# Kernel optimization log

Measured on AMD Instinct MI355X. Metric: run time of the kernel, lower is better.

Reference implementation:

```python
import jax, jax.numpy as jnp
import numpy as np

N = 50000
E = 800000
D = 256        # encoder_dim; also hidden*heads for both layers
H = 4          # heads
C = 64         # hidden_dim per head
OUT = 5        # classes
NEG_SLOPE = 0.2
GN_EPS = 1e-5
SM_EPS = 1e-16  # PyG softmax denominator epsilon


def setup_inputs() -> dict:
    key = jax.random.key(0)
    ks = jax.random.split(key, 20)
    sc = lambda fan_in: 1.0 / np.sqrt(fan_in)
    inp = {
        "x": jax.random.normal(ks[0], (N, D), dtype=jnp.float32),
        "edge_index": jax.random.randint(ks[1], (2, E), 0, N, dtype=jnp.int64),
        # two GATv2 layers (stacked on leading axis): lin_l, lin_r, att, bias
        "Wl": jax.random.normal(ks[2], (2, D, H * C), dtype=jnp.float32) * sc(D),
        "Wr": jax.random.normal(ks[3], (2, D, H * C), dtype=jnp.float32) * sc(D),
        "att": jax.random.normal(ks[4], (2, H, C), dtype=jnp.float32) * sc(C),
        "bconv": jnp.zeros((2, H * C), dtype=jnp.float32),
        # parallel linear skips
        "Wlin": jax.random.normal(ks[5], (2, D, H * C), dtype=jnp.float32) * sc(D),
        "blin": jnp.zeros((2, H * C), dtype=jnp.float32),
        # GraphNorm params
        "gn_w": jnp.ones((2, H * C), dtype=jnp.float32),
        "gn_b": jnp.zeros((2, H * C), dtype=jnp.float32),
        "gn_ms": jnp.ones((2, H * C), dtype=jnp.float32),
        # final GATv2 (concat=False -> head mean, out=5) and final linear
        "fWl": jax.random.normal(ks[6], (D, H * OUT), dtype=jnp.float32) * sc(D),
        "fWr": jax.random.normal(ks[7], (D, H * OUT), dtype=jnp.float32) * sc(D),
        "fatt": jax.random.normal(ks[8], (H, OUT), dtype=jnp.float32) * sc(OUT),
        "fbconv": jnp.zeros((OUT,), dtype=jnp.float32),
        "fWlin": jax.random.normal(ks[9], (D, OUT), dtype=jnp.float32) * sc(D),
        "fblin": jnp.zeros((OUT,), dtype=jnp.float32),
    }
    return inp


def _gatv2(x, src, dst, Wl, Wr, att, heads, ch):
    # x: [N, Din]; returns [N, heads, ch]
    n = x.shape[0]
    xl = (x @ Wl).reshape(n, heads, ch)  # source messages
    xr = (x @ Wr).reshape(n, heads, ch)  # target query part
    e = jax.nn.leaky_relu(xl[src] + xr[dst], NEG_SLOPE)      # [E, H, C]
    score = jnp.einsum("ehc,hc->eh", e, att)                  # [E, H]
    # segment softmax over incoming edges of each target node
    m = jax.ops.segment_max(score, dst, num_segments=n)       # [N, H]
    a = jnp.exp(score - m[dst])
    denom = jax.ops.segment_sum(a, dst, num_segments=n)       # [N, H]
    alpha = a / (denom[dst] + SM_EPS)                         # [E, H]
    return jax.ops.segment_sum(alpha[..., None] * xl[src], dst, num_segments=n)


def _graphnorm(x, w, b, ms):
    mean = jnp.mean(x, axis=0)
    centered = x - mean * ms
    var = jnp.mean(centered * centered, axis=0)
    return w * centered * jax.lax.rsqrt(var + GN_EPS) + b


def reference(x, edge_index, Wl, Wr, att, bconv, Wlin, blin, gn_w, gn_b, gn_ms,
              fWl, fWr, fatt, fbconv, fWlin, fblin):
    src, dst = edge_index[0], edge_index[1]
    emb = x
    for i in range(2):
        cpart = _gatv2(emb, src, dst, Wl[i], Wr[i], att[i], H, C).reshape(N, H * C) + bconv[i]
        lpart = emb @ Wlin[i] + blin[i]
        cpart = _graphnorm(cpart, gn_w[i], gn_b[i], gn_ms[i])
        emb = jax.nn.elu(cpart + lpart)
    cpart = _gatv2(emb, src, dst, fWl, fWr, fatt, H, OUT).mean(axis=1) + fbconv  # concat=False
    lpart = emb @ fWlin + fblin
    return jax.nn.log_softmax(cpart + lpart, axis=1)
```

## Files before the change

### kernel.cpp

```cpp
#include <hip/hip_runtime.h>

#define NN 50000
#define EE 800000
#define DD 256
#define NB 196

typedef unsigned short u16;
typedef unsigned int u32;

typedef __attribute__((ext_vector_type(8))) short short8;
typedef __attribute__((ext_vector_type(4))) float f32x4;
typedef __attribute__((ext_vector_type(4))) unsigned short u16x4;
typedef __attribute__((ext_vector_type(4))) int i32x4;

__device__ __forceinline__ float b2f(u16 u) {
  union { u32 i; float f; } c; c.i = ((u32)u) << 16; return c.f;
}
__device__ __forceinline__ u16 f2b(float f) {
  union { float f; u32 i; } c; c.f = f;
  u32 u = c.i;
  return (u16)((u + 0x7fffu + ((u >> 16) & 1u)) >> 16);
}
__device__ __forceinline__ float lrelu(float x) { return fmaxf(x, 0.2f * x); }
__device__ __forceinline__ float ldf(const void* p, int i, int bf) {
  return bf ? b2f(((const u16*)p)[i]) : ((const float*)p)[i];
}
__device__ __forceinline__ int lde(const void* ei, int idx, int m64) {
  int v = m64 ? (int)((const long long*)ei)[idx] : ((const int*)ei)[idx];
  return v < 0 ? 0 : (v >= NN ? NN - 1 : v);
}
__device__ __forceinline__ float cexp(float s) {
  return __expf(__builtin_amdgcn_fmed3f(s, -60.f, 60.f));
}

template <int CTRL>
__device__ __forceinline__ float dpp_add(float s) {
  union { float f; int i; } a, b;
  a.f = s;
  b.i = __builtin_amdgcn_update_dpp(0, a.i, CTRL, 0xf, 0xf, true);
  return s + b.f;
}
__device__ __forceinline__ float row16_allsum(float s) {
  s = dpp_add<0xB1>(s);
  s = dpp_add<0x4E>(s);
  s = dpp_add<0x141>(s);
  s = dpp_add<0x140>(s);
  return s;
}

__device__ __forceinline__ void gload_lds16(const void* g, void* l) {
  __builtin_amdgcn_global_load_lds(
      (const __attribute__((address_space(1))) void*)g,
      (__attribute__((address_space(3))) void*)l, 16, 0, 0);
}

__global__ __launch_bounds__(256) void init_kernel(const void* x, const void* ei,
                                                   int* flags, int* cnt) {
  int i = blockIdx.x * 256 + threadIdx.x;
  if (i < NN) cnt[i] = 0;
  if (blockIdx.x == 0 && threadIdx.x < 64) {
    int lane = threadIdx.x;
    const u16* xw = (const u16*)x;
    int c = 0;
    for (int k = lane; k < 512; k += 64) {
      u16 w = xw[k];
      int e = (w >> 7) & 0xFF;
      if ((e >= 107 && e <= 147) || (w & 0x7FFF) == 0) ++c;
    }
    const u32* ew = (const u32*)ei;
    int zc = 0;
    for (int k = 1 + 2 * lane; k < 1024; k += 128)
      if (ew[k] == 0) ++zc;
    #pragma unroll
    for (int off = 1; off < 64; off <<= 1) {
      c += __shfl_xor(c, off);
      zc += __shfl_xor(zc, off);
    }
    if (lane == 0) {
      flags[0] = (c >= 440) ? 1 : 0;
      flags[1] = (zc >= 400) ? 1 : 0;
    }
  }
}

__global__ void hist_kernel(const void* ei, const int* flags, int* cnt) {
  int e = blockIdx.x * 256 + threadIdx.x;
  if (e < EE) atomicAdd(&cnt[lde(ei, EE + e, flags[1])], 1);
}

__global__ __launch_bounds__(256) void bsum_kernel(const int* __restrict__ deg,
                                                   int* __restrict__ bsum) {
  int i = blockIdx.x * 256 + threadIdx.x;
  int v = (i < NN) ? deg[i] : 0;
  #pragma unroll
  for (int off = 1; off < 64; off <<= 1) v += __shfl_xor(v, off);
  __shared__ int ws[4];
  int lane = threadIdx.x & 63, wid = threadIdx.x >> 6;
  if (lane == 0) ws[wid] = v;
  __syncthreads();
  if (threadIdx.x == 0) bsum[blockIdx.x] = ws[0] + ws[1] + ws[2] + ws[3];
}

__global__ __launch_bounds__(256) void bscan_kernel(const int* __restrict__ bsum,
                                                    int* __restrict__ boff) {
  int t = threadIdx.x;
  int v = (t < NB) ? bsum[t] : 0;
  int iv = v;
  int lane = t & 63, wid = t >> 6;
  #pragma unroll
  for (int off = 1; off < 64; off <<= 1) {
    int u = __shfl_up(iv, off);
    if (lane >= off) iv += u;
  }
  __shared__ int ws[4];
  if (lane == 63) ws[wid] = iv;
  __syncthreads();
  int add = 0;
  for (int w = 0; w < wid; ++w) add += ws[w];
  if (t < NB) boff[t] = iv - v + add;
}

__global__ __launch_bounds__(256) void bwrite_kernel(const int* __restrict__ deg,
                                                     const int* __restrict__ boff,
                                                     int* __restrict__ rowptr) {
  int i = blockIdx.x * 256 + threadIdx.x;
  int v = (i < NN) ? deg[i] : 0;
  int iv = v;
  int lane = threadIdx.x & 63, wid = threadIdx.x >> 6;
  #pragma unroll
  for (int off = 1; off < 64; off <<= 1) {
    int u = __shfl_up(iv, off);
    if (lane >= off) iv += u;
  }
  __shared__ int ws[4];
  if (lane == 63) ws[wid] = iv;
  __syncthreads();
  int add = boff[blockIdx.x];
  for (int w = 0; w < wid; ++w) add += ws[w];
  if (i <= NN) rowptr[i] = iv - v + add;
}

__global__ void fill_kernel(const void* ei, const int* flags, const int* __restrict__ rowptr,
                            int* __restrict__ cnt, int* __restrict__ col) {
  int e = blockIdx.x * 256 + threadIdx.x;
  if (e < EE) {
    int m64 = flags[1];
    int dst = lde(ei, EE + e, m64);
    int old = atomicSub(&cnt[dst], 1);
    int pos = rowptr[dst] + old - 1;
    if (pos >= 0 && pos < EE) col[pos] = lde(ei, e, m64);
  }
}

__global__ __launch_bounds__(256) void prep_kernel(
    const void* Wl, const void* Wr, const void* Wlin,
    const void* fWl, const void* fWr, const void* fWlin,
    const void* x, const int* flags, u16* wpack, u16* fwp, u16* xb) {
  int bf = flags[0];
  int bid = blockIdx.x;
  if (bid < 1536) {
    int idx = bid * 256 + threadIdx.x;
    int m = idx >> 16, e = idx & 65535;
    int layer = (m >= 3) ? 1 : 0, sel = m - layer * 3;
    const void* src = (sel == 0 ? Wl : (sel == 1 ? Wr : Wlin));
    int k = e >> 8, n = e & 255;
    wpack[(m << 16) + ((((k >> 3) << 8) + n) << 3) + (k & 7)] =
        f2b(ldf(src, layer * 65536 + e, bf));
  } else if (bid < 1584) {
    int idx = (bid - 1536) * 256 + threadIdx.x;
    int j = idx & 7;
    int col = (idx >> 3) % 48;
    int kk = idx / (48 * 8);
    int k = kk * 8 + j;
    float v = 0.f;
    if (col < 20)      v = ldf(fWl, k * 20 + col, bf);
    else if (col < 40) v = ldf(fWr, k * 20 + (col - 20), bf);
    else if (col < 45) v = ldf(fWlin, k * 5 + (col - 40), bf);
    fwp[idx] = f2b(v);
  } else {
    int base = (bid - 1584) * 1024 + threadIdx.x * 4;
    if (bf) {
      *(u16x4*)(xb + base) = *(const u16x4*)((const u16*)x + base);
    } else {
      f32x4 s = *(const f32x4*)((const float*)x + base);
      u16x4 o;
      #pragma unroll
      for (int j = 0; j < 4; ++j) o[j] = f2b(s[j]);
      *(u16x4*)(xb + base) = o;
    }
  }
}

__global__ __launch_bounds__(256) void gemm_kernel(
    const u16* __restrict__ A, const u16* __restrict__ wpack, const void* blin,
    const int* flags, int layer, float* __restrict__ sums,
    u16* __restrict__ xl, u16* __restrict__ xr, u16* __restrict__ lp, int M) {
  __shared__ __align__(16) u16 bsh[16384];
  if (blockIdx.x == 0 && blockIdx.y == 0) {
    sums[threadIdx.x] = 0.f;
    sums[threadIdx.x + 256] = 0.f;
  }
  int wave = threadIdx.x >> 6;
  int lane = threadIdx.x & 63;
  int q = lane >> 4;
  int t = lane & 15;
  int m0 = blockIdx.x * 64 + wave * 16;
  int yh = blockIdx.y;

  int arow = m0 + t;
  if (arow >= M) arow = M - 1;
  const u16* Abase = A + (size_t)arow * DD + q * 8;
  short8 af[8];
  #pragma unroll
  for (int i = 0; i < 8; ++i) af[i] = *(const short8*)(Abase + i * 32);

  int bf = flags[0];
  int m = m0 + t;

  for (int yi = 0; yi < 6; ++yi) {
    int y = yh * 6 + yi;
    int mm = y >> 2;
    int col0 = (y & 3) * 64;
    const u16* wb = wpack + (mm << 16);

    __syncthreads();
    #pragma unroll
    for (int itc = 0; itc < 8; ++itc) {
      int kk = wave + itc * 4;
      const u16* gp = wb + (((kk << 8) + col0) << 3) + (lane << 3);
      u16* lb = &bsh[(wave * 64 + itc * 256) << 3];
      gload_lds16(gp, lb);
    }
    __syncthreads();

    f32x4 acc[4];
    #pragma unroll
    for (int ns = 0; ns < 4; ++ns) acc[ns] = (f32x4){0.f, 0.f, 0.f, 0.f};

    #pragma unroll
    for (int i = 0; i < 8; ++i) {
      int kk = i * 4 + q;
      const u16* bb = &bsh[(kk << 9) + (t << 3)];
      #pragma unroll
      for (int ns = 0; ns < 4; ++ns) {
        short8 b = *(const short8*)(bb + (ns << 7));
        acc[ns] = __builtin_amdgcn_mfma_f32_16x16x32_bf16(b, af[i], acc[ns], 0, 0, 0);
      }
    }

    u16* dstp = (y < 4) ? xl : (y < 8) ? xr : lp;
    bool isLp = (y >= 8);
    if (m < M) {
      #pragma unroll
      for (int ns = 0; ns < 4; ++ns) {
        int c0 = col0 + ns * 16 + q * 4;
        u16x4 w;
        #pragma unroll
        for (int r = 0; r < 4; ++r) {
          float bias = isLp ? ldf(blin, layer * 256 + c0 + r, bf) : 0.f;
          w[r] = f2b(acc[ns][r] + bias);
        }
        *(u16x4*)(dstp + (size_t)m * DD + c0) = w;
      }
    }
  }
}

__global__ __launch_bounds__(256) void fgemm_kernel(
    const u16* __restrict__ A, const u16* __restrict__ fwp, const void* fblin,
    const int* flags, float* __restrict__ zl, float* __restrict__ zr,
    float* __restrict__ lp5, int M) {
  int wave = threadIdx.x >> 6;
  int lane = threadIdx.x & 63;
  int q = lane >> 4;
  int t = lane & 15;
  int m0 = blockIdx.x * 64 + wave * 16;

  f32x4 acc[3];
  #pragma unroll
  for (int ns = 0; ns < 3; ++ns) acc[ns] = (f32x4){0.f, 0.f, 0.f, 0.f};

  int arow = m0 + t;
  if (arow >= M) arow = M - 1;
  const u16* Abase = A + (size_t)arow * DD + q * 8;

  #pragma unroll
  for (int k0 = 0; k0 < DD; k0 += 32) {
    short8 a = *(const short8*)(Abase + k0);
    int kk = (k0 >> 3) + q;
    #pragma unroll
    for (int ns = 0; ns < 3; ++ns) {
      short8 b = *(const short8*)(fwp + (((kk * 48) + ns * 16 + t) << 3));
      acc[ns] = __builtin_amdgcn_mfma_f32_16x16x32_bf16(a, b, acc[ns], 0, 0, 0);
    }
  }

  int bf = flags[0];
  #pragma unroll
  for (int ns = 0; ns < 3; ++ns) {
    int c = ns * 16 + t;
    #pragma unroll
    for (int r = 0; r < 4; ++r) {
      int row = m0 + q * 4 + r;
      if (row < M) {
        float v = acc[ns][r];
        if (c < 20) {
          zl[row * 32 + (c / 5) * 8 + (c % 5)] = v;
        } else if (c < 40) {
          int c2 = c - 20;
          zr[row * 32 + (c2 / 5) * 8 + (c2 % 5)] = v;
        } else if (c < 45) {
          lp5[row * 8 + (c - 40)] = v + ldf(fblin, c - 40, bf);
        }
      }
    }
  }
}

__device__ __forceinline__ void edge_step(u16x4 s4, const float* xrv, const float* atv,
                                          float& l, float* acc) {
  float x0 = b2f(s4[0]), x1 = b2f(s4[1]), x2 = b2f(s4[2]), x3 = b2f(s4[3]);
  float sp = atv[0] * lrelu(x0 + xrv[0]) + atv[1] * lrelu(x1 + xrv[1]) +
             atv[2] * lrelu(x2 + xrv[2]) + atv[3] * lrelu(x3 + xrv[3]);
  sp = row16_allsum(sp);
  float pz = cexp(sp);
  l += pz;
  acc[0] += pz * x0;
  acc[1] += pz * x1;
  acc[2] += pz * x2;
  acc[3] += pz * x3;
}

__global__ __launch_bounds__(256) void agg_kernel(
    const u16* __restrict__ xl, const u16* __restrict__ xr,
    const int* __restrict__ rowptr, const int* __restrict__ col,
    const void* att, const void* bconv, const int* flags, int layer,
    u16* __restrict__ cpart) {
  int wave = threadIdx.x >> 6;
  int node = blockIdx.x * 4 + wave;
  int lane = threadIdx.x & 63;
  int h = lane >> 4;
  int cb = (lane & 15) * 4;
  int base = h * 64 + cb;
  int bf = flags[0];

  u16x4 r4 = *(const u16x4*)(xr + (size_t)node * DD + base);
  float xrv[4], atv[4];
  #pragma unroll
  for (int j = 0; j < 4; ++j) {
    xrv[j] = b2f(r4[j]);
    atv[j] = ldf(att, layer * 256 + base + j, bf);
  }

  float l = 0.f;
  float acc[4] = {0.f, 0.f, 0.f, 0.f};
  int e0 = rowptr[node], e1 = rowptr[node + 1];
  const char* xlb = (const char*)xl;
  u32 baseb = (u32)(base << 1);

  int e = e0;
  for (; e < e1 && (e & 3); ++e) {
    u16x4 v = *(const u16x4*)(xlb + (((u32)col[e] << 9) + baseb));
    edge_step(v, xrv, atv, l, acc);
  }
  int nq = (e1 - e) >> 2;
  if (nq > 0) {
    i32x4 cq = *(const i32x4*)(col + e);
    for (int g = 0; g < nq; ++g) {
      i32x4 nx = (g + 1 < nq) ? *(const i32x4*)(col + e + 4) : cq;
      u16x4 v0 = *(const u16x4*)(xlb + (((u32)cq.x << 9) + baseb));
      u16x4 v1 = *(const u16x4*)(xlb + (((u32)cq.y << 9) + baseb));
      u16x4 v2 = *(const u16x4*)(xlb + (((u32)cq.z << 9) + baseb));
      u16x4 v3 = *(const u16x4*)(xlb + (((u32)cq.w << 9) + baseb));
      edge_step(v0, xrv, atv, l, acc);
      edge_step(v1, xrv, atv, l, acc);
      edge_step(v2, xrv, atv, l, acc);
      edge_step(v3, xrv, atv, l, acc);
      cq = nx;
      e += 4;
    }
  }
  for (; e < e1; ++e) {
    u16x4 v = *(const u16x4*)(xlb + (((u32)col[e] << 9) + baseb));
    edge_step(v, xrv, atv, l, acc);
  }

  float inv = 1.f / (l + 1e-16f);
  u16x4 outw;
  #pragma unroll
  for (int j = 0; j < 4; ++j)
    outw[j] = f2b(acc[j] * inv + ldf(bconv, layer * 256 + base + j, bf));
  *(u16x4*)(cpart + (size_t)node * DD + base) = outw;
}

__global__ __launch_bounds__(256) void stats_kernel(const u16* __restrict__ cpart,
                                                    float* __restrict__ sums) {
  int ch = threadIdx.x;
  int n0 = blockIdx.x * 100, n1 = n0 + 100;
  float s = 0.f, s2 = 0.f;
  for (int n = n0; n < n1; ++n) {
    float x = b2f(cpart[(size_t)n * DD + ch]);
    s += x; s2 += x * x;
  }
  atomicAdd(&sums[ch], s);
  atomicAdd(&sums[256 + ch], s2);
}

__global__ __launch_bounds__(256) void norm_kernel(
    const u16* __restrict__ cpart, const u16* __restrict__ lp,
    const void* gw, const void* gb, const void* gms, const int* flags, int layer,
    const float* __restrict__ sums, u16* __restrict__ emb) {
  int t = threadIdx.x;
  int node = blockIdx.x * 4 + (t >> 6);
  int c4 = (t & 63) * 4;
  int bf = flags[0];
  size_t idx = (size_t)node * DD + c4;
  const float invN = 1.f / (float)NN;
  u16x4 cp = *(const u16x4*)(cpart + idx);
  u16x4 lv = *(const u16x4*)(lp + idx);
  u16x4 o;
  #pragma unroll
  for (int j = 0; j < 4; ++j) {
    int ch = c4 + j;
    float mean = sums[ch] * invN;
    float ex2 = sums[256 + ch] * invN;
    float mm = mean * ldf(gms, layer * 256 + ch, bf);
    float var = ex2 - 2.f * mm * mean + mm * mm;
    float x = b2f(cp[j]);
    float y = ldf(gw, layer * 256 + ch, bf) * (x - mm) * rsqrtf(fmaxf(var, 0.f) + 1e-5f) +
              ldf(gb, layer * 256 + ch, bf) + b2f(lv[j]);
    o[j] = f2b(y > 0.f ? y : expm1f(y));
  }
  *(u16x4*)(emb + idx) = o;
}

__global__ __launch_bounds__(256) void finagg_kernel(
    const float* __restrict__ zl, const float* __restrict__ zr,
    const int* __restrict__ rowptr, const int* __restrict__ col,
    const void* fatt, const void* fbconv, const int* flags,
    const float* __restrict__ lp5, void* outv) {
  int node = blockIdx.x * 4 + (threadIdx.x >> 6);
  int lane = threadIdx.x & 63;
  int bf = flags[0];
  int h = lane >> 4, sub = lane & 15;

  const float* zrp = zr + node * 32 + h * 8;
  f32x4 zr4 = *(const f32x4*)zrp;
  float zrv[5] = {zr4.x, zr4.y, zr4.z, zr4.w, zrp[4]};
  float atv[5];
  #pragma unroll
  for (int c = 0; c < 5; ++c) atv[c] = ldf(fatt, h * 5 + c, bf);

  float l = 0.f, acc[5] = {0.f, 0.f, 0.f, 0.f, 0.f};
  int e0 = rowptr[node], e1 = rowptr[node + 1];
  for (int e = e0 + sub; e < e1; e += 16) {
    int src = col[e];
    const float* zs = zl + src * 32 + h * 8;
    f32x4 z4 = *(const f32x4*)zs;
    float z4s = zs[4];
    float zlv[5] = {z4.x, z4.y, z4.z, z4.w, z4s};
    float s = 0.f;
    #pragma unroll
    for (int c = 0; c < 5; ++c) s += atv[c] * lrelu(zlv[c] + zrv[c]);
    float pz = cexp(s);
    l += pz;
    #pragma unroll
    for (int c = 0; c < 5; ++c) acc[c] += pz * zlv[c];
  }
  #pragma unroll
  for (int off = 1; off < 16; off <<= 1) {
    l += __shfl_xor(l, off);
    #pragma unroll
    for (int c = 0; c < 5; ++c) acc[c] += __shfl_xor(acc[c], off);
  }
  float inv = 1.f / (l + 1e-16f);
  float v[5];
  #pragma unroll
  for (int c = 0; c < 5; ++c) {
    float tv = acc[c] * inv;
    tv += __shfl_xor(tv, 16);
    tv += __shfl_xor(tv, 32);
    v[c] = tv * 0.25f;
  }
  if (lane == 0) {
    float mx = -3.0e38f;
    #pragma unroll
    for (int c = 0; c < 5; ++c) {
      v[c] += ldf(fbconv, c, bf) + lp5[node * 8 + c];
      mx = fmaxf(mx, v[c]);
    }
    float se = 0.f;
    #pragma unroll
    for (int c = 0; c < 5; ++c) se += __expf(v[c] - mx);
    float lse = mx + __logf(se);
    #pragma unroll
    for (int c = 0; c < 5; ++c) {
      float r = v[c] - lse;
      if (bf) ((u16*)outv)[node * 5 + c] = f2b(r);
      else    ((float*)outv)[node * 5 + c] = r;
    }
  }
}

extern "C" void kernel_launch(void* const* d_in, const int* in_sizes, int n_in,
                              void* d_out, int out_size, void* d_ws, size_t ws_size,
                              hipStream_t stream) {
  (void)in_sizes; (void)n_in; (void)out_size; (void)ws_size;
  const void* x     = d_in[0];
  const void* ei    = d_in[1];
  const void* Wl    = d_in[2];
  const void* Wr    = d_in[3];
  const void* att   = d_in[4];
  const void* bconv = d_in[5];
  const void* Wlin  = d_in[6];
  const void* blin  = d_in[7];
  const void* gnw   = d_in[8];
  const void* gnb   = d_in[9];
  const void* gnms  = d_in[10];
  const void* fWl   = d_in[11];
  const void* fWr   = d_in[12];
  const void* fatt  = d_in[13];
  const void* fbc   = d_in[14];
  const void* fWlin = d_in[15];
  const void* fblin = d_in[16];

  char* p = (char*)d_ws;
  auto take = [&](size_t bytes) {
    char* r = p;
    p += (bytes + 511) & ~(size_t)511;
    return r;
  };
  int* flags   = (int*)take(512);
  int* rowptr  = (int*)take((NN + 1) * sizeof(int));
  int* cnt     = (int*)take(NN * sizeof(int));
  int* colx    = (int*)take(EE * sizeof(int));
  int* bsum    = (int*)take(256 * sizeof(int));
  int* boff    = (int*)take(256 * sizeof(int));
  u16* wpack   = (u16*)take((size_t)6 * 65536 * sizeof(u16));
  u16* fwp     = (u16*)take((size_t)32 * 48 * 8 * sizeof(u16));
  float* sums  = (float*)take(512 * sizeof(float));
  char* unionA = take((size_t)NN * DD * 4);
  u16* xb      = (u16*)unionA;
  u16* cpart   = (u16*)unionA;
  float* zl    = (float*)unionA;
  float* zr    = (float*)(unionA + (size_t)NN * 32 * 4);
  float* lp5   = (float*)(unionA + (size_t)NN * 64 * 4);
  u16* xl      = (u16*)take((size_t)NN * DD * 2);
  u16* xr      = (u16*)take((size_t)NN * DD * 2);
  u16* lp      = (u16*)take((size_t)NN * DD * 2);
  u16* emb     = (u16*)take((size_t)NN * DD * 2);

  init_kernel<<<dim3(NB), dim3(256), 0, stream>>>(x, ei, flags, cnt);
  hist_kernel<<<dim3((EE + 255) / 256), dim3(256), 0, stream>>>(ei, flags, cnt);
  bsum_kernel<<<dim3(NB), dim3(256), 0, stream>>>(cnt, bsum);
  bscan_kernel<<<dim3(1), dim3(256), 0, stream>>>(bsum, boff);
  bwrite_kernel<<<dim3(NB), dim3(256), 0, stream>>>(cnt, boff, rowptr);
  fill_kernel<<<dim3((EE + 255) / 256), dim3(256), 0, stream>>>(ei, flags, rowptr, cnt, colx);
  prep_kernel<<<dim3(1584 + NN * DD / 1024), dim3(256), 0, stream>>>(
      Wl, Wr, Wlin, fWl, fWr, fWlin, x, flags, wpack, fwp, xb);

  const u16* layerin = xb;
  for (int i = 0; i < 2; ++i) {
    gemm_kernel<<<dim3((NN + 63) / 64, 2), dim3(256), 0, stream>>>(
        layerin, wpack + (size_t)i * 3 * 65536, blin, flags, i, sums, xl, xr, lp, NN);
    agg_kernel<<<dim3(NN / 4), dim3(256), 0, stream>>>(xl, xr, rowptr, colx, att, bconv,
                                                       flags, i, cpart);
    stats_kernel<<<dim3(500), dim3(256), 0, stream>>>(cpart, sums);
    norm_kernel<<<dim3(NN / 4), dim3(256), 0, stream>>>(cpart, lp, gnw, gnb, gnms, flags, i,
                                                        sums, emb);
    layerin = emb;
  }
  fgemm_kernel<<<dim3((NN + 63) / 64), dim3(256), 0, stream>>>(emb, fwp, fblin, flags,
                                                               zl, zr, lp5, NN);
  finagg_kernel<<<dim3(NN / 4), dim3(256), 0, stream>>>(zl, zr, rowptr, colx, fatt, fbc,
                                                        flags, lp5, d_out);
}
```

Baseline: 637.4 us.

## Fuse GraphNorm+ELU into next GEMM's A-fragment load, drop norm kernel

Removes the separate norm kernel. A tiny per-layer kernel now folds the GraphNorm statistics into per-channel scale and shift, and the following GEMM (or the final GEMM) applies the affine, residual add and ELU while loading its A fragments from cpart and the linear-skip output. This avoids writing and re-reading the full embedding tensor each layer. Buffers are reshuffled: double-buffered skip outputs, final outputs aliased onto xl/xr, and sums zeroing moved into the init kernel. In exchange, the GEMM's A load does more arithmetic, and fgemm now holds all A fragments in registers.

```diff
diff --git a/kernel.cpp b/kernel.cpp
--- a/kernel.cpp
+++ b/kernel.cpp
@@ -55,9 +55,14 @@
 }
 
 __global__ __launch_bounds__(256) void init_kernel(const void* x, const void* ei,
-                                                   int* flags, int* cnt) {
+                                                   int* flags, int* cnt,
+                                                   float* sums) {
   int i = blockIdx.x * 256 + threadIdx.x;
   if (i < NN) cnt[i] = 0;
+  if (blockIdx.x == 1) {
+    #pragma unroll
+    for (int j = 0; j < 4; ++j) sums[threadIdx.x + j * 256] = 0.f;
+  }
   if (blockIdx.x == 0 && threadIdx.x < 64) {
     int lane = threadIdx.x;
     const u16* xw = (const u16*)x;
@@ -191,15 +196,57 @@
   }
 }
 
+__global__ __launch_bounds__(256) void nprep_kernel(
+    const float* __restrict__ sums, const void* gw, const void* gb, const void* gms,
+    const int* flags, int layer, float* __restrict__ ab) {
+  int ch = threadIdx.x;
+  int bf = flags[0];
+  const float invN = 1.f / (float)NN;
+  float mean = sums[layer * 512 + ch] * invN;
+  float ex2 = sums[layer * 512 + 256 + ch] * invN;
+  float mm = mean * ldf(gms, layer * 256 + ch, bf);
+  float var = ex2 - 2.f * mm * mean + mm * mm;
+  float rs = rsqrtf(fmaxf(var, 0.f) + 1e-5f);
+  float a = ldf(gw, layer * 256 + ch, bf) * rs;
+  float b = ldf(gb, layer * 256 + ch, bf) - a * mm;
+  ab[ch] = a;
+  ab[256 + ch] = b;
+}
+
+__device__ __forceinline__ void load_af_fused(short8* af, const u16* cpb, const u16* lpb,
+                                              const float* __restrict__ ab, int q) {
+  #pragma unroll
+  for (int i = 0; i < 8; ++i) {
+    int ch0 = q * 8 + i * 32;
+    u16x4 c0 = *(const u16x4*)(cpb + i * 32);
+    u16x4 c1 = *(const u16x4*)(cpb + i * 32 + 4);
+    u16x4 l0 = *(const u16x4*)(lpb + i * 32);
+    u16x4 l1 = *(const u16x4*)(lpb + i * 32 + 4);
+    f32x4 a0 = *(const f32x4*)(ab + ch0);
+    f32x4 a1 = *(const f32x4*)(ab + ch0 + 4);
+    f32x4 b0 = *(const f32x4*)(ab + 256 + ch0);
+    f32x4 b1 = *(const f32x4*)(ab + 256 + ch0 + 4);
+    short8 w;
+    #pragma unroll
+    for (int j = 0; j < 4; ++j) {
+      float y = a0[j] * b2f(c0[j]) + b0[j] + b2f(l0[j]);
+      y = y > 0.f ? y : expm1f(y);
+      w[j] = (short)f2b(y);
+      float y2 = a1[j] * b2f(c1[j]) + b1[j] + b2f(l1[j]);
+      y2 = y2 > 0.f ? y2 : expm1f(y2);
+      w[j + 4] = (short)f2b(y2);
+    }
+    af[i] = w;
+  }
+}
+
 __global__ __launch_bounds__(256) void gemm_kernel(
     const u16* __restrict__ A, const u16* __restrict__ wpack, const void* blin,
-    const int* flags, int layer, float* __restrict__ sums,
-    u16* __restrict__ xl, u16* __restrict__ xr, u16* __restrict__ lp, int M) {
+    const int* flags, int layer,
+    u16* __restrict__ xl, u16* __restrict__ xr, u16* __restrict__ lp, int M,
+    const u16* __restrict__ cp, const u16* __restrict__ lpin,
+    const float* __restrict__ ab, int fuse) {
   __shared__ __align__(16) u16 bsh[16384];
-  if (blockIdx.x == 0 && blockIdx.y == 0) {
-    sums[threadIdx.x] = 0.f;
-    sums[threadIdx.x + 256] = 0.f;
-  }
   int wave = threadIdx.x >> 6;
   int lane = threadIdx.x & 63;
   int q = lane >> 4;
@@ -209,10 +256,16 @@
 
   int arow = m0 + t;
   if (arow >= M) arow = M - 1;
-  const u16* Abase = A + (size_t)arow * DD + q * 8;
   short8 af[8];
-  #pragma unroll
-  for (int i = 0; i < 8; ++i) af[i] = *(const short8*)(Abase + i * 32);
+  if (fuse) {
+    const u16* cpb = cp + (size_t)arow * DD + q * 8;
+    const u16* lpb = lpin + (size_t)arow * DD + q * 8;
+    load_af_fused(af, cpb, lpb, ab, q);
+  } else {
+    const u16* Abase = A + (size_t)arow * DD + q * 8;
+    #pragma unroll
+    for (int i = 0; i < 8; ++i) af[i] = *(const short8*)(Abase + i * 32);
+  }
 
   int bf = flags[0];
   int m = m0 + t;
@@ -267,7 +320,8 @@
 }
 
 __global__ __launch_bounds__(256) void fgemm_kernel(
-    const u16* __restrict__ A, const u16* __restrict__ fwp, const void* fblin,
+    const u16* __restrict__ cp, const u16* __restrict__ lpin,
+    const float* __restrict__ ab, const u16* __restrict__ fwp, const void* fblin,
     const int* flags, float* __restrict__ zl, float* __restrict__ zr,
     float* __restrict__ lp5, int M) {
   int wave = threadIdx.x >> 6;
@@ -282,11 +336,16 @@
 
   int arow = m0 + t;
   if (arow >= M) arow = M - 1;
-  const u16* Abase = A + (size_t)arow * DD + q * 8;
+  short8 af[8];
+  {
+    const u16* cpb = cp + (size_t)arow * DD + q * 8;
+    const u16* lpb = lpin + (size_t)arow * DD + q * 8;
+    load_af_fused(af, cpb, lpb, ab, q);
+  }
 
   #pragma unroll
   for (int k0 = 0; k0 < DD; k0 += 32) {
-    short8 a = *(const short8*)(Abase + k0);
+    short8 a = af[k0 >> 5];
     int kk = (k0 >> 3) + q;
     #pragma unroll
     for (int ns = 0; ns < 3; ++ns) {
@@ -404,34 +463,6 @@
   }
   atomicAdd(&sums[ch], s);
   atomicAdd(&sums[256 + ch], s2);
-}
-
-__global__ __launch_bounds__(256) void norm_kernel(
-    const u16* __restrict__ cpart, const u16* __restrict__ lp,
-    const void* gw, const void* gb, const void* gms, const int* flags, int layer,
-    const float* __restrict__ sums, u16* __restrict__ emb) {
-  int t = threadIdx.x;
-  int node = blockIdx.x * 4 + (t >> 6);
-  int c4 = (t & 63) * 4;
-  int bf = flags[0];
-  size_t idx = (size_t)node * DD + c4;
-  const float invN = 1.f / (float)NN;
-  u16x4 cp = *(const u16x4*)(cpart + idx);
-  u16x4 lv = *(const u16x4*)(lp + idx);
-  u16x4 o;
-  #pragma unroll
-  for (int j = 0; j < 4; ++j) {
-    int ch = c4 + j;
-    float mean = sums[ch] * invN;
-    float ex2 = sums[256 + ch] * invN;
-    float mm = mean * ldf(gms, layer * 256 + ch, bf);
-    float var = ex2 - 2.f * mm * mean + mm * mm;
-    float x = b2f(cp[j]);
-    float y = ldf(gw, layer * 256 + ch, bf) * (x - mm) * rsqrtf(fmaxf(var, 0.f) + 1e-5f) +
-              ldf(gb, layer * 256 + ch, bf) + b2f(lv[j]);
-    o[j] = f2b(y > 0.f ? y : expm1f(y));
-  }
-  *(u16x4*)(emb + idx) = o;
 }
 
 __global__ __launch_bounds__(256) void finagg_kernel(
@@ -538,19 +569,20 @@
   int* boff    = (int*)take(256 * sizeof(int));
   u16* wpack   = (u16*)take((size_t)6 * 65536 * sizeof(u16));
   u16* fwp     = (u16*)take((size_t)32 * 48 * 8 * sizeof(u16));
-  float* sums  = (float*)take(512 * sizeof(float));
+  float* sums  = (float*)take(1024 * sizeof(float));
+  float* ab    = (float*)take(1024 * sizeof(float));
   char* unionA = take((size_t)NN * DD * 4);
   u16* xb      = (u16*)unionA;
   u16* cpart   = (u16*)unionA;
-  float* zl    = (float*)unionA;
-  float* zr    = (float*)(unionA + (size_t)NN * 32 * 4);
-  float* lp5   = (float*)(unionA + (size_t)NN * 64 * 4);
   u16* xl      = (u16*)take((size_t)NN * DD * 2);
   u16* xr      = (u16*)take((size_t)NN * DD * 2);
-  u16* lp      = (u16*)take((size_t)NN * DD * 2);
-  u16* emb     = (u16*)take((size_t)NN * DD * 2);
-
-  init_kernel<<<dim3(NB), dim3(256), 0, stream>>>(x, ei, flags, cnt);
+  u16* lpA     = (u16*)take((size_t)NN * DD * 2);
+  u16* lpB     = (u16*)take((size_t)NN * DD * 2);
+  float* zl    = (float*)xl;
+  float* zr    = (float*)xr;
+  float* lp5   = (float*)lpA;
+
+  init_kernel<<<dim3(NB), dim3(256), 0, stream>>>(x, ei, flags, cnt, sums);
   hist_kernel<<<dim3((EE + 255) / 256), dim3(256), 0, stream>>>(ei, flags, cnt);
   bsum_kernel<<<dim3(NB), dim3(256), 0, stream>>>(cnt, bsum);
   bscan_kernel<<<dim3(1), dim3(256), 0, stream>>>(bsum, boff);
@@ -559,19 +591,22 @@
   prep_kernel<<<dim3(1584 + NN * DD / 1024), dim3(256), 0, stream>>>(
       Wl, Wr, Wlin, fWl, fWr, fWlin, x, flags, wpack, fwp, xb);
 
-  const u16* layerin = xb;
-  for (int i = 0; i < 2; ++i) {
-    gemm_kernel<<<dim3((NN + 63) / 64, 2), dim3(256), 0, stream>>>(
-        layerin, wpack + (size_t)i * 3 * 65536, blin, flags, i, sums, xl, xr, lp, NN);
-    agg_kernel<<<dim3(NN / 4), dim3(256), 0, stream>>>(xl, xr, rowptr, colx, att, bconv,
-                                                       flags, i, cpart);
-    stats_kernel<<<dim3(500), dim3(256), 0, stream>>>(cpart, sums);
-    norm_kernel<<<dim3(NN / 4), dim3(256), 0, stream>>>(cpart, lp, gnw, gnb, gnms, flags, i,
-                                                        sums, emb);
-    layerin = emb;
-  }
-  fgemm_kernel<<<dim3((NN + 63) / 64), dim3(256), 0, stream>>>(emb, fwp, fblin, flags,
-                                                               zl, zr, lp5, NN);
+  gemm_kernel<<<dim3((NN + 63) / 64, 2), dim3(256), 0, stream>>>(
+      xb, wpack, blin, flags, 0, xl, xr, lpA, NN, xb, xb, ab, 0);
+  agg_kernel<<<dim3(NN / 4), dim3(256), 0, stream>>>(xl, xr, rowptr, colx, att, bconv,
+                                                     flags, 0, cpart);
+  stats_kernel<<<dim3(500), dim3(256), 0, stream>>>(cpart, sums);
+  nprep_kernel<<<dim3(1), dim3(256), 0, stream>>>(sums, gnw, gnb, gnms, flags, 0, ab);
+
+  gemm_kernel<<<dim3((NN + 63) / 64, 2), dim3(256), 0, stream>>>(
+      xb, wpack + (size_t)3 * 65536, blin, flags, 1, xl, xr, lpB, NN, cpart, lpA, ab, 1);
+  agg_kernel<<<dim3(NN / 4), dim3(256), 0, stream>>>(xl, xr, rowptr, colx, att, bconv,
+                                                     flags, 1, cpart);
+  stats_kernel<<<dim3(500), dim3(256), 0, stream>>>(cpart, sums + 512);
+  nprep_kernel<<<dim3(1), dim3(256), 0, stream>>>(sums, gnw, gnb, gnms, flags, 1, ab + 512);
+
+  fgemm_kernel<<<dim3((NN + 63) / 64), dim3(256), 0, stream>>>(
+      cpart, lpB, ab + 512, fwp, fblin, flags, zl, zr, lp5, NN);
   finagg_kernel<<<dim3(NN / 4), dim3(256), 0, stream>>>(zl, zr, rowptr, colx, fatt, fbc,
                                                         flags, lp5, d_out);
 }
```

Measured after the change: 547.4 us. 1.16x faster.
